# Performance work log

Measured on AMD Instinct MI355X. Metric: run time of the kernel, lower is better.

Reference implementation:

```python
import jax, jax.numpy as jnp
import numpy as np

NSLICES = 4
HID = 512
IN_FEAT = 342   # input_shape - 1 (last column is phase)
OUT = 311
BATCH = 256


def cubic(y0, y1, y2, y3, mu):
    # Catmull-Rom cubic interpolation, as in the original PFNN code
    return (
        (-0.5 * y0 + 1.5 * y1 - 1.5 * y2 + 0.5 * y3) * mu * mu * mu
        + (y0 - 2.5 * y1 + 2.0 * y2 - 0.5 * y3) * mu * mu
        + (-0.5 * y0 + 0.5 * y2) * mu
        + y1
    )


def setup_inputs() -> dict:
    key = jax.random.key(0)
    ks = jax.random.split(key, 7)
    x = jax.random.uniform(ks[0], (BATCH, IN_FEAT + 1), dtype=jnp.float32)
    s = 0.02
    W0 = jax.random.normal(ks[1], (NSLICES, HID, IN_FEAT), dtype=jnp.float32) * s
    b0 = jax.random.normal(ks[2], (NSLICES, HID), dtype=jnp.float32) * s
    W1 = jax.random.normal(ks[3], (NSLICES, HID, HID), dtype=jnp.float32) * s
    b1 = jax.random.normal(ks[4], (NSLICES, HID), dtype=jnp.float32) * s
    W2 = jax.random.normal(ks[5], (NSLICES, OUT, HID), dtype=jnp.float32) * s
    b2 = jax.random.normal(ks[6], (NSLICES, OUT), dtype=jnp.float32) * s
    return {"x": x, "W0": W0, "b0": b0, "W1": W1, "b1": b1, "W2": W2, "b2": b2}


def reference(x, W0, b0, W1, b1, W2, b2):
    phase = x[:, -1]                       # [B]
    pscale = NSLICES * phase
    mu = jnp.mod(pscale, 1.0)              # [B]
    i1 = jnp.floor(pscale).astype(jnp.int32) % NSLICES
    i0 = (i1 - 1) % NSLICES
    i2 = (i1 + 1) % NSLICES
    i3 = (i1 + 2) % NSLICES
    muW = mu[:, None, None]                # broadcast over (out, in)
    mub = mu[:, None]

    Wb0 = cubic(W0[i0], W0[i1], W0[i2], W0[i3], muW)   # [B, 512, 342]
    bb0 = cubic(b0[i0], b0[i1], b0[i2], b0[i3], mub)   # [B, 512]
    Wb1 = cubic(W1[i0], W1[i1], W1[i2], W1[i3], muW)   # [B, 512, 512]
    bb1 = cubic(b1[i0], b1[i1], b1[i2], b1[i3], mub)
    Wb2 = cubic(W2[i0], W2[i1], W2[i2], W2[i3], muW)   # [B, 311, 512]
    bb2 = cubic(b2[i0], b2[i1], b2[i2], b2[i3], mub)

    h = x[:, :-1]                                       # [B, 342]
    h = jax.nn.elu(jnp.einsum('boi,bi->bo', Wb0, h) + bb0)
    h = jax.nn.elu(jnp.einsum('boi,bi->bo', Wb1, h) + bb1)
    out = jnp.einsum('boi,bi->bo', Wb2, h) + bb2        # [B, 311]
    return out
```

## Files before the change

### kernel.cpp

```cpp
#include <hip/hip_runtime.h>
#include <math.h>

#define HID 512
#define IN_FEAT 342
#define OUTD 311
#define BATCH 256
#define KP0 352
#define MP2 320
#define XROW (IN_FEAT + 1)

typedef unsigned short u16;
typedef short bf16x8 __attribute__((ext_vector_type(8)));
typedef float f32x4 __attribute__((ext_vector_type(4)));

__device__ __forceinline__ u16 f2bf_rne(float v) {
    unsigned int x = __float_as_uint(v);
    unsigned int r = (x + 0x7fffu + ((x >> 16) & 1u)) >> 16;
    return (u16)r;
}
__device__ __forceinline__ float bf2f(u16 u) {
    return __uint_as_float(((unsigned int)u) << 16);
}

#define C0 (4 * 512 * 44)
#define C1 (4 * 512 * 64)
#define C2 (4 * 320 * 64)
#define CX (256 * 44)
#define PREP_TOT (C0 + C1 + C2 + CX + 256)

union U8 { u16 u[8]; uint4 v; };

__global__ __launch_bounds__(256) void prep_all(
    const float* __restrict__ x,
    const float* __restrict__ W0, const float* __restrict__ W1, const float* __restrict__ W2,
    u16* __restrict__ whi0, u16* __restrict__ wlo0,
    u16* __restrict__ whi1, u16* __restrict__ wlo1,
    u16* __restrict__ whi2, u16* __restrict__ wlo2,
    u16* __restrict__ h0hi, u16* __restrict__ h0lo,
    float* __restrict__ dcoef)
{
    int i = blockIdx.x * 256 + threadIdx.x;
    if (i >= PREP_TOT) return;

    if (i >= C0 + C1 + C2 + CX) {
        int b = i - (C0 + C1 + C2 + CX);
        float ps = 4.f * x[(size_t)b * XROW + IN_FEAT];
        float fl = floorf(ps);
        float mu = ps - fl;
        int i1 = ((int)fl) & 3;
        float mu2 = mu * mu, mu3 = mu2 * mu;
        float c0 = -0.5f * mu3 + mu2 - 0.5f * mu;
        float c1 = 1.5f * mu3 - 2.5f * mu2 + 1.0f;
        float c2 = -1.5f * mu3 + 2.0f * mu2 + 0.5f * mu;
        float c3 = 0.5f * mu3 - 0.5f * mu2;
        float d[4];
        d[(i1 + 3) & 3] = c0;
        d[i1]           = c1;
        d[(i1 + 1) & 3] = c2;
        d[(i1 + 2) & 3] = c3;
        *reinterpret_cast<float4*>(dcoef + b * 4) = make_float4(d[0], d[1], d[2], d[3]);
        return;
    }

    float src[8];
    u16 *dhi, *dlo; size_t doff;
    if (i < C0) {
        int row = i / 44, c = i - row * 44;
        int k = c * 8;
#pragma unroll
        for (int j = 0; j < 8; j++) {
            int kk = k + j;
            src[j] = (kk < IN_FEAT) ? W0[(size_t)row * IN_FEAT + kk] : 0.f;
        }
        dhi = whi0; dlo = wlo0; doff = (size_t)row * KP0 + k;
    } else if (i < C0 + C1) {
        int l = i - C0;
        int row = l >> 6, c = l & 63;
        int k = c * 8;
        const float* p = W1 + (size_t)row * HID + k;
#pragma unroll
        for (int j = 0; j < 8; j++) src[j] = p[j];
        dhi = whi1; dlo = wlo1; doff = (size_t)row * HID + k;
    } else if (i < C0 + C1 + C2) {
        int l = i - C0 - C1;
        int row = l >> 6, c = l & 63;
        int k = c * 8;
        int s = row / 320, o = row - s * 320;
        if (o < OUTD) {
            const float* p = W2 + ((size_t)s * OUTD + o) * HID + k;
#pragma unroll
            for (int j = 0; j < 8; j++) src[j] = p[j];
        } else {
#pragma unroll
            for (int j = 0; j < 8; j++) src[j] = 0.f;
        }
        dhi = whi2; dlo = wlo2; doff = (size_t)row * HID + k;
    } else {
        int l = i - C0 - C1 - C2;
        int b = l / 44, c = l - b * 44;
        int k = c * 8;
#pragma unroll
        for (int j = 0; j < 8; j++) {
            int kk = k + j;
            src[j] = (kk < IN_FEAT) ? x[(size_t)b * XROW + kk] : 0.f;
        }
        dhi = h0hi; dlo = h0lo; doff = (size_t)b * KP0 + k;
    }

    U8 hi, lo;
#pragma unroll
    for (int j = 0; j < 8; j++) {
        u16 h = f2bf_rne(src[j]);
        hi.u[j] = h;
        lo.u[j] = f2bf_rne(src[j] - bf2f(h));
    }
    *reinterpret_cast<uint4*>(dhi + doff) = hi.v;
    *reinterpret_cast<uint4*>(dlo + doff) = lo.v;
}

template<int KP, int KLDS, int NB, int FINAL>
__global__ __launch_bounds__(NB * 16, (NB == 16 ? 2 : 1)) void layer_v3(
    const u16* __restrict__ Whi, const u16* __restrict__ Wlo, int Mp,
    const u16* __restrict__ Hhi, const u16* __restrict__ Hlo,
    const float* __restrict__ bias, const float* __restrict__ dcoef, int Mb,
    u16* __restrict__ Ohi, u16* __restrict__ Olo, float* __restrict__ outp)
{
    union SharedU {
        u16 h[2][NB * KLDS];
        float acc[4][NB][17];
    };
    __shared__ SharedU sm;

    const int tid = (int)threadIdx.x;
    const int b0 = (int)blockIdx.x * NB;
    const int o0 = (int)blockIdx.y * 16;
    constexpr int NTHR = NB * 16;

    constexpr int CH = KP / 8;
    for (int idx = tid; idx < NB * CH; idx += NTHR) {
        int r = idx / CH, c = idx - r * CH;
        size_t g = (size_t)(b0 + r) * KP + c * 8;
        *reinterpret_cast<uint4*>(&sm.h[0][r * KLDS + c * 8]) =
            *reinterpret_cast<const uint4*>(Hhi + g);
        *reinterpret_cast<uint4*>(&sm.h[1][r * KLDS + c * 8]) =
            *reinterpret_cast<const uint4*>(Hlo + g);
    }
    __syncthreads();

    const int lane = tid & 63;
    const int w = tid >> 6;
    const int s = w & 3;
    const int t = w >> 2;
    const int m = lane & 15;
    const int q = lane >> 4;

    const size_t wro = ((size_t)s * Mp + o0 + m) * KP + q * 8;
    const u16* wph = Whi + wro;
    const u16* wpl = Wlo + wro;
    const u16* hp = &sm.h[0][(t * 16 + m) * KLDS + q * 8];

    f32x4 a0 = {0.f, 0.f, 0.f, 0.f};
    f32x4 a1 = {0.f, 0.f, 0.f, 0.f};
    f32x4 a2 = {0.f, 0.f, 0.f, 0.f};
#pragma unroll
    for (int cc = 0; cc < KP / 32; ++cc) {
        bf16x8 ah = *reinterpret_cast<const bf16x8*>(wph + cc * 32);
        bf16x8 al = *reinterpret_cast<const bf16x8*>(wpl + cc * 32);
        bf16x8 bh = *reinterpret_cast<const bf16x8*>(hp + cc * 32);
        bf16x8 bl = *reinterpret_cast<const bf16x8*>(hp + cc * 32 + NB * KLDS);
        a0 = __builtin_amdgcn_mfma_f32_16x16x32_bf16(ah, bh, a0, 0, 0, 0);
        a1 = __builtin_amdgcn_mfma_f32_16x16x32_bf16(ah, bl, a1, 0, 0, 0);
        a2 = __builtin_amdgcn_mfma_f32_16x16x32_bf16(al, bh, a2, 0, 0, 0);
    }
    __syncthreads();

    const float ds = dcoef[(size_t)(b0 + t * 16 + m) * 4 + s];
    f32x4 sum = a0 + a1 + a2;
#pragma unroll
    for (int r = 0; r < 4; ++r) {
        int o = o0 + q * 4 + r;
        float bb = (o < Mb) ? bias[(size_t)s * Mb + o] : 0.f;
        sm.acc[s][t * 16 + m][q * 4 + r] = ds * (sum[r] + bb);
    }
    __syncthreads();

    const int b_l = tid >> 4;
    const int o_l = tid & 15;
    float vv = sm.acc[0][b_l][o_l] + sm.acc[1][b_l][o_l]
             + sm.acc[2][b_l][o_l] + sm.acc[3][b_l][o_l];
    const int o = o0 + o_l;
    const int b = b0 + b_l;
    if (!FINAL) {
        float e = (vv > 0.f) ? vv : expm1f(vv);
        u16 h = f2bf_rne(e);
        Ohi[(size_t)b * HID + o] = h;
        Olo[(size_t)b * HID + o] = f2bf_rne(e - bf2f(h));
    } else if (o < OUTD) {
        outp[(size_t)b * OUTD + o] = vv;
    }
}

extern "C" void kernel_launch(void* const* d_in, const int* in_sizes, int n_in,
                              void* d_out, int out_size, void* d_ws, size_t ws_size,
                              hipStream_t stream) {
    const float* x  = (const float*)d_in[0];
    const float* W0 = (const float*)d_in[1];
    const float* b0 = (const float*)d_in[2];
    const float* W1 = (const float*)d_in[3];
    const float* b1 = (const float*)d_in[4];
    const float* W2 = (const float*)d_in[5];
    const float* b2 = (const float*)d_in[6];
    float* out = (float*)d_out;

    char* pw = (char*)d_ws;
    auto alloc = [&](size_t bytes) { char* r = pw; pw += (bytes + 255) & ~(size_t)255; return r; };

    float* dcoef = (float*)alloc(BATCH * 4 * sizeof(float));
    u16* whi0 = (u16*)alloc((size_t)4 * HID * KP0 * 2);
    u16* wlo0 = (u16*)alloc((size_t)4 * HID * KP0 * 2);
    u16* whi1 = (u16*)alloc((size_t)4 * HID * HID * 2);
    u16* wlo1 = (u16*)alloc((size_t)4 * HID * HID * 2);
    u16* whi2 = (u16*)alloc((size_t)4 * MP2 * HID * 2);
    u16* wlo2 = (u16*)alloc((size_t)4 * MP2 * HID * 2);
    u16* h0hi = (u16*)alloc((size_t)BATCH * KP0 * 2);
    u16* h0lo = (u16*)alloc((size_t)BATCH * KP0 * 2);
    u16* hahi = (u16*)alloc((size_t)BATCH * HID * 2);
    u16* halo = (u16*)alloc((size_t)BATCH * HID * 2);
    u16* hbhi = (u16*)alloc((size_t)BATCH * HID * 2);
    u16* hblo = (u16*)alloc((size_t)BATCH * HID * 2);

    prep_all<<<dim3((PREP_TOT + 255) / 256), 256, 0, stream>>>(
        x, W0, W1, W2, whi0, wlo0, whi1, wlo1, whi2, wlo2, h0hi, h0lo, dcoef);

    layer_v3<KP0, 360, 32, 0><<<dim3(BATCH / 32, HID / 16), 512, 0, stream>>>(
        whi0, wlo0, HID, h0hi, h0lo, b0, dcoef, HID, hahi, halo, nullptr);

    layer_v3<HID, 520, 32, 0><<<dim3(BATCH / 32, HID / 16), 512, 0, stream>>>(
        whi1, wlo1, HID, hahi, halo, b1, dcoef, HID, hbhi, hblo, nullptr);

    layer_v3<HID, 520, 16, 1><<<dim3(BATCH / 16, MP2 / 16), 256, 0, stream>>>(
        whi2, wlo2, MP2, hbhi, hblo, b2, dcoef, OUTD, nullptr, nullptr, out);
}
```

Before: 102.9 us.

## Fuse weight bf16 split and phase coefficients into layer kernels, drop prep pass

Removes the separate prep kernel that converted all weights and the input into hi/lo bf16 buffers and precomputed Catmull-Rom coefficients. Each layer kernel now reads fp32 weights directly, splits them to hi/lo bf16 in registers before the MFMA, converts x to bf16 in the first layer's LDS load, and computes its per-row phase coefficient inline. This saves one launch and the write-then-reread of the converted weight buffers. In exchange each weight element is read as fp32, twice the bytes of the old bf16 pair reads per block, and converted redundantly by every batch-tile block.

```diff
diff --git a/kernel.cpp b/kernel.cpp
--- a/kernel.cpp
+++ b/kernel.cpp
@@ -22,109 +22,24 @@
     return __uint_as_float(((unsigned int)u) << 16);
 }
 
-#define C0 (4 * 512 * 44)
-#define C1 (4 * 512 * 64)
-#define C2 (4 * 320 * 64)
-#define CX (256 * 44)
-#define PREP_TOT (C0 + C1 + C2 + CX + 256)
-
-union U8 { u16 u[8]; uint4 v; };
-
-__global__ __launch_bounds__(256) void prep_all(
-    const float* __restrict__ x,
-    const float* __restrict__ W0, const float* __restrict__ W1, const float* __restrict__ W2,
-    u16* __restrict__ whi0, u16* __restrict__ wlo0,
-    u16* __restrict__ whi1, u16* __restrict__ wlo1,
-    u16* __restrict__ whi2, u16* __restrict__ wlo2,
-    u16* __restrict__ h0hi, u16* __restrict__ h0lo,
-    float* __restrict__ dcoef)
-{
-    int i = blockIdx.x * 256 + threadIdx.x;
-    if (i >= PREP_TOT) return;
-
-    if (i >= C0 + C1 + C2 + CX) {
-        int b = i - (C0 + C1 + C2 + CX);
-        float ps = 4.f * x[(size_t)b * XROW + IN_FEAT];
-        float fl = floorf(ps);
-        float mu = ps - fl;
-        int i1 = ((int)fl) & 3;
-        float mu2 = mu * mu, mu3 = mu2 * mu;
-        float c0 = -0.5f * mu3 + mu2 - 0.5f * mu;
-        float c1 = 1.5f * mu3 - 2.5f * mu2 + 1.0f;
-        float c2 = -1.5f * mu3 + 2.0f * mu2 + 0.5f * mu;
-        float c3 = 0.5f * mu3 - 0.5f * mu2;
-        float d[4];
-        d[(i1 + 3) & 3] = c0;
-        d[i1]           = c1;
-        d[(i1 + 1) & 3] = c2;
-        d[(i1 + 2) & 3] = c3;
-        *reinterpret_cast<float4*>(dcoef + b * 4) = make_float4(d[0], d[1], d[2], d[3]);
-        return;
-    }
-
-    float src[8];
-    u16 *dhi, *dlo; size_t doff;
-    if (i < C0) {
-        int row = i / 44, c = i - row * 44;
-        int k = c * 8;
-#pragma unroll
-        for (int j = 0; j < 8; j++) {
-            int kk = k + j;
-            src[j] = (kk < IN_FEAT) ? W0[(size_t)row * IN_FEAT + kk] : 0.f;
-        }
-        dhi = whi0; dlo = wlo0; doff = (size_t)row * KP0 + k;
-    } else if (i < C0 + C1) {
-        int l = i - C0;
-        int row = l >> 6, c = l & 63;
-        int k = c * 8;
-        const float* p = W1 + (size_t)row * HID + k;
-#pragma unroll
-        for (int j = 0; j < 8; j++) src[j] = p[j];
-        dhi = whi1; dlo = wlo1; doff = (size_t)row * HID + k;
-    } else if (i < C0 + C1 + C2) {
-        int l = i - C0 - C1;
-        int row = l >> 6, c = l & 63;
-        int k = c * 8;
-        int s = row / 320, o = row - s * 320;
-        if (o < OUTD) {
-            const float* p = W2 + ((size_t)s * OUTD + o) * HID + k;
-#pragma unroll
-            for (int j = 0; j < 8; j++) src[j] = p[j];
-        } else {
-#pragma unroll
-            for (int j = 0; j < 8; j++) src[j] = 0.f;
-        }
-        dhi = whi2; dlo = wlo2; doff = (size_t)row * HID + k;
-    } else {
-        int l = i - C0 - C1 - C2;
-        int b = l / 44, c = l - b * 44;
-        int k = c * 8;
-#pragma unroll
-        for (int j = 0; j < 8; j++) {
-            int kk = k + j;
-            src[j] = (kk < IN_FEAT) ? x[(size_t)b * XROW + kk] : 0.f;
-        }
-        dhi = h0hi; dlo = h0lo; doff = (size_t)b * KP0 + k;
-    }
-
-    U8 hi, lo;
+__device__ __forceinline__ void split8(const float* __restrict__ src, bf16x8& hi, bf16x8& lo) {
 #pragma unroll
     for (int j = 0; j < 8; j++) {
         u16 h = f2bf_rne(src[j]);
-        hi.u[j] = h;
-        lo.u[j] = f2bf_rne(src[j] - bf2f(h));
+        hi[j] = (short)h;
+        lo[j] = (short)f2bf_rne(src[j] - bf2f(h));
     }
-    *reinterpret_cast<uint4*>(dhi + doff) = hi.v;
-    *reinterpret_cast<uint4*>(dlo + doff) = lo.v;
 }
 
-template<int KP, int KLDS, int NB, int FINAL>
-__global__ __launch_bounds__(NB * 16, (NB == 16 ? 2 : 1)) void layer_v3(
-    const u16* __restrict__ Whi, const u16* __restrict__ Wlo, int Mp,
+template<int KP, int KLDS, int NB, int FINAL, int MODE, int KW, int MW>
+__global__ __launch_bounds__(NB * 16, (NB == 16 ? 2 : 1)) void layer_f32w(
+    const float* __restrict__ W,
+    const float* __restrict__ x,
     const u16* __restrict__ Hhi, const u16* __restrict__ Hlo,
-    const float* __restrict__ bias, const float* __restrict__ dcoef, int Mb,
+    const float* __restrict__ bias, int Mb,
     u16* __restrict__ Ohi, u16* __restrict__ Olo, float* __restrict__ outp)
 {
+    constexpr int NTHR = NB * 16;
     union SharedU {
         u16 h[2][NB * KLDS];
         float acc[4][NB][17];
@@ -134,16 +49,33 @@
     const int tid = (int)threadIdx.x;
     const int b0 = (int)blockIdx.x * NB;
     const int o0 = (int)blockIdx.y * 16;
-    constexpr int NTHR = NB * 16;
 
     constexpr int CH = KP / 8;
-    for (int idx = tid; idx < NB * CH; idx += NTHR) {
-        int r = idx / CH, c = idx - r * CH;
-        size_t g = (size_t)(b0 + r) * KP + c * 8;
-        *reinterpret_cast<uint4*>(&sm.h[0][r * KLDS + c * 8]) =
-            *reinterpret_cast<const uint4*>(Hhi + g);
-        *reinterpret_cast<uint4*>(&sm.h[1][r * KLDS + c * 8]) =
-            *reinterpret_cast<const uint4*>(Hlo + g);
+    if constexpr (MODE == 0) {
+        for (int idx = tid; idx < NB * CH; idx += NTHR) {
+            int r = idx / CH, c = idx - r * CH;
+            int k = c * 8;
+            const float* xr = x + (size_t)(b0 + r) * XROW;
+            float src[8];
+#pragma unroll
+            for (int j = 0; j < 8; j++) {
+                int kk = k + j;
+                src[j] = (kk < IN_FEAT) ? xr[kk] : 0.f;
+            }
+            bf16x8 hi, lo;
+            split8(src, hi, lo);
+            *reinterpret_cast<bf16x8*>(&sm.h[0][r * KLDS + k]) = hi;
+            *reinterpret_cast<bf16x8*>(&sm.h[1][r * KLDS + k]) = lo;
+        }
+    } else {
+        for (int idx = tid; idx < NB * CH; idx += NTHR) {
+            int r = idx / CH, c = idx - r * CH;
+            size_t g = (size_t)(b0 + r) * KP + c * 8;
+            *reinterpret_cast<uint4*>(&sm.h[0][r * KLDS + c * 8]) =
+                *reinterpret_cast<const uint4*>(Hhi + g);
+            *reinterpret_cast<uint4*>(&sm.h[1][r * KLDS + c * 8]) =
+                *reinterpret_cast<const uint4*>(Hlo + g);
+        }
     }
     __syncthreads();
 
@@ -154,18 +86,51 @@
     const int m = lane & 15;
     const int q = lane >> 4;
 
-    const size_t wro = ((size_t)s * Mp + o0 + m) * KP + q * 8;
-    const u16* wph = Whi + wro;
-    const u16* wpl = Wlo + wro;
+    const int orow = o0 + m;
+    const bool vrow = (MW == HID) ? true : (orow < MW);
+    const float* wr = W + ((size_t)s * MW + (vrow ? orow : 0)) * KW;
     const u16* hp = &sm.h[0][(t * 16 + m) * KLDS + q * 8];
+
+    const int brow = b0 + t * 16 + m;
+    const float ps = 4.f * x[(size_t)brow * XROW + IN_FEAT];
+    const float fl = floorf(ps);
+    const float mu = ps - fl;
+    const int i1 = ((int)fl) & 3;
+    const int jj = (s - i1) & 3;
+    const float mu2 = mu * mu, mu3 = mu2 * mu;
+    const float ds = (jj == 0) ? ( 1.5f * mu3 - 2.5f * mu2 + 1.0f)
+                   : (jj == 1) ? (-1.5f * mu3 + 2.0f * mu2 + 0.5f * mu)
+                   : (jj == 2) ? ( 0.5f * mu3 - 0.5f * mu2)
+                   :             (-0.5f * mu3 + mu2 - 0.5f * mu);
 
     f32x4 a0 = {0.f, 0.f, 0.f, 0.f};
     f32x4 a1 = {0.f, 0.f, 0.f, 0.f};
     f32x4 a2 = {0.f, 0.f, 0.f, 0.f};
 #pragma unroll
     for (int cc = 0; cc < KP / 32; ++cc) {
-        bf16x8 ah = *reinterpret_cast<const bf16x8*>(wph + cc * 32);
-        bf16x8 al = *reinterpret_cast<const bf16x8*>(wpl + cc * 32);
+        const int k0 = cc * 32 + q * 8;
+        float ws[8];
+        if (vrow && (cc * 32 + 32 <= KW)) {
+            if constexpr (KW % 4 == 0) {
+                const float4* p = reinterpret_cast<const float4*>(wr + k0);
+                float4 v0 = p[0], v1 = p[1];
+                ws[0] = v0.x; ws[1] = v0.y; ws[2] = v0.z; ws[3] = v0.w;
+                ws[4] = v1.x; ws[5] = v1.y; ws[6] = v1.z; ws[7] = v1.w;
+            } else {
+                const float2* p = reinterpret_cast<const float2*>(wr + k0);
+                float2 v0 = p[0], v1 = p[1], v2 = p[2], v3 = p[3];
+                ws[0] = v0.x; ws[1] = v0.y; ws[2] = v1.x; ws[3] = v1.y;
+                ws[4] = v2.x; ws[5] = v2.y; ws[6] = v3.x; ws[7] = v3.y;
+            }
+        } else {
+#pragma unroll
+            for (int j = 0; j < 8; j++) {
+                int kk = k0 + j;
+                ws[j] = (vrow && kk < KW) ? wr[kk] : 0.f;
+            }
+        }
+        bf16x8 ah, al;
+        split8(ws, ah, al);
         bf16x8 bh = *reinterpret_cast<const bf16x8*>(hp + cc * 32);
         bf16x8 bl = *reinterpret_cast<const bf16x8*>(hp + cc * 32 + NB * KLDS);
         a0 = __builtin_amdgcn_mfma_f32_16x16x32_bf16(ah, bh, a0, 0, 0, 0);
@@ -174,7 +139,6 @@
     }
     __syncthreads();
 
-    const float ds = dcoef[(size_t)(b0 + t * 16 + m) * 4 + s];
     f32x4 sum = a0 + a1 + a2;
 #pragma unroll
     for (int r = 0; r < 4; ++r) {
@@ -205,39 +169,27 @@
                               hipStream_t stream) {
     const float* x  = (const float*)d_in[0];
     const float* W0 = (const float*)d_in[1];
-    const float* b0 = (const float*)d_in[2];
+    const float* b0v = (const float*)d_in[2];
     const float* W1 = (const float*)d_in[3];
-    const float* b1 = (const float*)d_in[4];
+    const float* b1v = (const float*)d_in[4];
     const float* W2 = (const float*)d_in[5];
-    const float* b2 = (const float*)d_in[6];
+    const float* b2v = (const float*)d_in[6];
     float* out = (float*)d_out;
 
     char* pw = (char*)d_ws;
     auto alloc = [&](size_t bytes) { char* r = pw; pw += (bytes + 255) & ~(size_t)255; return r; };
 
-    float* dcoef = (float*)alloc(BATCH * 4 * sizeof(float));
-    u16* whi0 = (u16*)alloc((size_t)4 * HID * KP0 * 2);
-    u16* wlo0 = (u16*)alloc((size_t)4 * HID * KP0 * 2);
-    u16* whi1 = (u16*)alloc((size_t)4 * HID * HID * 2);
-    u16* wlo1 = (u16*)alloc((size_t)4 * HID * HID * 2);
-    u16* whi2 = (u16*)alloc((size_t)4 * MP2 * HID * 2);
-    u16* wlo2 = (u16*)alloc((size_t)4 * MP2 * HID * 2);
-    u16* h0hi = (u16*)alloc((size_t)BATCH * KP0 * 2);
-    u16* h0lo = (u16*)alloc((size_t)BATCH * KP0 * 2);
     u16* hahi = (u16*)alloc((size_t)BATCH * HID * 2);
     u16* halo = (u16*)alloc((size_t)BATCH * HID * 2);
     u16* hbhi = (u16*)alloc((size_t)BATCH * HID * 2);
     u16* hblo = (u16*)alloc((size_t)BATCH * HID * 2);
 
-    prep_all<<<dim3((PREP_TOT + 255) / 256), 256, 0, stream>>>(
-        x, W0, W1, W2, whi0, wlo0, whi1, wlo1, whi2, wlo2, h0hi, h0lo, dcoef);
+    layer_f32w<KP0, 360, 32, 0, 0, IN_FEAT, HID><<<dim3(BATCH / 32, HID / 16), 512, 0, stream>>>(
+        W0, x, nullptr, nullptr, b0v, HID, hahi, halo, nullptr);
 
-    layer_v3<KP0, 360, 32, 0><<<dim3(BATCH / 32, HID / 16), 512, 0, stream>>>(
-        whi0, wlo0, HID, h0hi, h0lo, b0, dcoef, HID, hahi, halo, nullptr);
+    layer_f32w<HID, 520, 32, 0, 1, HID, HID><<<dim3(BATCH / 32, HID / 16), 512, 0, stream>>>(
+        W1, x, hahi, halo, b1v, HID, hbhi, hblo, nullptr);
 
-    layer_v3<HID, 520, 32, 0><<<dim3(BATCH / 32, HID / 16), 512, 0, stream>>>(
-        whi1, wlo1, HID, hahi, halo, b1, dcoef, HID, hbhi, hblo, nullptr);
-
-    layer_v3<HID, 520, 16, 1><<<dim3(BATCH / 16, MP2 / 16), 256, 0, stream>>>(
-        whi2, wlo2, MP2, hbhi, hblo, b2, dcoef, OUTD, nullptr, nullptr, out);
+    layer_f32w<HID, 520, 16, 1, 1, HID, OUTD><<<dim3(BATCH / 16, MP2 / 16), 256, 0, stream>>>(
+        W2, x, hbhi, hblo, b2v, OUTD, nullptr, nullptr, out);
 }
```

Result: no change. 104.9 us (+1.9%).
